# Kernel tuning notes

Measured on AMD Instinct MI355X. Metric: run time of the kernel, lower is better.

The kernel has to match this reference:

```python
import jax, jax.numpy as jnp
import numpy as np

N = 100000
E = 3200000
F_IN, F1, F2, F3, FB, NC = 256, 64, 32, 16, 8, 10


def setup_inputs() -> dict:
    key = jax.random.key(0)
    ks = jax.random.split(key, 12)
    features = jax.random.normal(ks[0], (N, F_IN), dtype=jnp.float32)
    edge_index = jax.random.randint(ks[1], (2, E), 0, N, dtype=jnp.int64)
    def glorot(k, shape):
        lim = np.sqrt(6.0 / (shape[0] + shape[1]))
        return jax.random.uniform(k, shape, jnp.float32, -lim, lim)
    return {
        "features": features,
        "edge_index": edge_index,
        "W1": glorot(ks[2], (F_IN, F1)), "b1": jnp.zeros((F1,), jnp.float32),
        "W2": glorot(ks[3], (F1, F2)),  "b2": jnp.zeros((F2,), jnp.float32),
        "W3": glorot(ks[4], (F2, F3)),  "b3": jnp.zeros((F3,), jnp.float32),
        "Wf": glorot(ks[5], (F3, FB)),  "bf": jnp.zeros((FB,), jnp.float32),
        "Ws": glorot(ks[6], (FB, NC)),  "bs": jnp.zeros((NC,), jnp.float32),
    }


def _gcn_norm(edge_index, n):
    # symmetric normalization with self-loops: deg includes +1 for self-loop
    src, dst = edge_index[0], edge_index[1]
    ones = jnp.ones((edge_index.shape[1],), jnp.float32)
    deg = jax.ops.segment_sum(ones, dst, num_segments=n) + 1.0
    dinv = jax.lax.rsqrt(deg)
    edge_w = dinv[src] * dinv[dst]        # [E]
    self_w = dinv * dinv                   # [N], self-loop weight
    return src, dst, edge_w, self_w


def _gcn_conv(x, W, b, src, dst, edge_w, self_w, n):
    xw = x @ W                                         # [N, Fout]
    msg = xw[src] * edge_w[:, None]                    # gather + scale
    agg = jax.ops.segment_sum(msg, dst, num_segments=n)
    return agg + xw * self_w[:, None] + b


def reference(features, edge_index, W1, b1, W2, b2, W3, b3, Wf, bf, Ws, bs):
    n = features.shape[0]
    src, dst, edge_w, self_w = _gcn_norm(edge_index, n)
    h = jax.nn.relu(_gcn_conv(features, W1, b1, src, dst, edge_w, self_w, n))
    h = jax.nn.relu(_gcn_conv(h, W2, b2, src, dst, edge_w, self_w, n))
    h = jax.nn.relu(_gcn_conv(h, W3, b3, src, dst, edge_w, self_w, n))
    pooled = jnp.mean(h, axis=0, keepdims=True)        # [1, F3]
    hidden = jax.nn.relu(pooled @ Wf + bf)
    scores = hidden @ Ws + bs
    return jax.nn.log_softmax(scores, axis=1)
```

## Files before the change

### kernel.cpp

```cpp
#include <hip/hip_runtime.h>
#include <hip/hip_fp16.h>
#include <math.h>

#define TPB 256
#define BKT_SHIFT 9
#define BKT_N 512
#define NB_MAX 256
#define CHUNK 4096
#define CAP   24576
#define Y_SCALE 16.0f
#define Y_INV_SCALE (1.0f / 16.0f)

typedef short bf16x8 __attribute__((ext_vector_type(8)));
typedef float f32x4  __attribute__((ext_vector_type(4)));

static __device__ inline unsigned short f2bf(float f) {
    union { float f; unsigned u; } v; v.f = f;
    unsigned r = v.u + 0x7FFF + ((v.u >> 16) & 1);
    return (unsigned short)(r >> 16);
}

static __device__ inline unsigned char f2fp8(float x) {
    int p = __builtin_amdgcn_cvt_pk_fp8_f32(x, x, 0, false);
    return (unsigned char)(p & 0xFF);
}

static __device__ inline void acc_word(float* a, unsigned u) {
    a[0] += __builtin_amdgcn_cvt_f32_fp8(u, 0);
    a[1] += __builtin_amdgcn_cvt_f32_fp8(u, 1);
    a[2] += __builtin_amdgcn_cvt_f32_fp8(u, 2);
    a[3] += __builtin_amdgcn_cvt_f32_fp8(u, 3);
}

__global__ __launch_bounds__(256) void setup_kernel(
    const float* __restrict__ W1, unsigned short* __restrict__ Wt1,
    const float* __restrict__ W2, unsigned short* __restrict__ Wt2,
    const float* __restrict__ W3, unsigned short* __restrict__ Wt3,
    int* __restrict__ bcursor, float* __restrict__ pooled, int nbkt)
{
    const int b = blockIdx.x;
    if (b < 16) {
        int base = b * 1024;
        for (int i = base + threadIdx.x; i < base + 1024; i += 256) {
            int k = i / 64, c = i % 64;
            Wt1[c * 256 + k] = f2bf(W1[i]);
        }
    } else if (b < 18) {
        int base = (b - 16) * 1024;
        for (int i = base + threadIdx.x; i < base + 1024; i += 256) {
            int k = i / 32, c = i % 32;
            Wt2[c * 64 + k] = f2bf(W2[i]);
        }
    } else if (b == 18) {
        for (int i = threadIdx.x; i < 512; i += 256) {
            int k = i / 16, c = i % 16;
            Wt3[c * 32 + k] = f2bf(W3[i]);
        }
    } else {
        if (threadIdx.x < nbkt) bcursor[threadIdx.x] = threadIdx.x * CAP;
        if (threadIdx.x < 16) pooled[threadIdx.x] = 0.f;
    }
}

__global__ __launch_bounds__(TPB) void bucket_scatter(
    const int* __restrict__ src, const int* __restrict__ dst,
    int* __restrict__ bcursor, unsigned int* __restrict__ packed, int E, int nbkt)
{
    __shared__ unsigned int  spk[CHUNK];
    __shared__ unsigned char sbk[CHUNK];
    __shared__ int h[NB_MAX];
    __shared__ int base[NB_MAX];
    for (int c0 = blockIdx.x * CHUNK; c0 < E; c0 += gridDim.x * CHUNK) {
        int m = min(CHUNK, E - c0);
        for (int i = threadIdx.x; i < nbkt; i += TPB) h[i] = 0;
        __syncthreads();
        for (int i = threadIdx.x; i < m; i += TPB) {
            int d = dst[c0 + i];
            int s = src[c0 + i];
            int b = d >> BKT_SHIFT;
            spk[i] = ((unsigned)(d & (BKT_N - 1)) << 17) | (unsigned)s;
            sbk[i] = (unsigned char)b;
            atomicAdd(&h[b], 1);
        }
        __syncthreads();
        for (int i = threadIdx.x; i < nbkt; i += TPB) {
            int c = h[i];
            base[i] = c ? atomicAdd(&bcursor[i], c) : 0;
            h[i] = 0;
        }
        __syncthreads();
        for (int i = threadIdx.x; i < m; i += TPB) {
            int b = sbk[i];
            int pos = base[b] + atomicAdd(&h[b], 1);
            packed[pos] = spk[i];
        }
        __syncthreads();
    }
}

__global__ __launch_bounds__(256) void bucket_offsets(
    const int* __restrict__ bcursor, int* __restrict__ boff, int nbkt, int E)
{
    int t = threadIdx.x;
    int v = (t < nbkt) ? (bcursor[t] - t * CAP) : 0;
    __shared__ int tmp[256];
    tmp[t] = v; __syncthreads();
    for (int s = 1; s < 256; s <<= 1) {
        int x = (t >= s) ? tmp[t - s] : 0;
        __syncthreads();
        tmp[t] += x;
        __syncthreads();
    }
    if (t < nbkt) boff[t] = tmp[t] - v;
    if (t == 0) boff[nbkt] = E;
}

__global__ __launch_bounds__(256) void bucket_csr(
    const unsigned int* __restrict__ packed, const int* __restrict__ boff,
    int* __restrict__ off, float* __restrict__ dinv, int* __restrict__ ssrc,
    int n, int nbkt)
{
    const int b   = blockIdx.x;
    const int e0  = boff[b];
    const int cnt = boff[b + 1] - e0;
    const int p0  = b * CAP;
    const int v0  = b << BKT_SHIFT;
    const int nv  = min(BKT_N, n - v0);
    const int t   = threadIdx.x;

    __shared__ int hist[BKT_N];
    __shared__ int cur[BKT_N];
    __shared__ int tmp[256];

    for (int i = t; i < nv; i += 256) hist[i] = 0;
    __syncthreads();
    for (int e = t; e < cnt; e += 256)
        atomicAdd(&hist[packed[p0 + e] >> 17], 1);
    __syncthreads();

    int a = (2 * t     < nv) ? hist[2 * t]     : 0;
    int c = (2 * t + 1 < nv) ? hist[2 * t + 1] : 0;
    int ps = a + c;
    tmp[t] = ps; __syncthreads();
    for (int s = 1; s < 256; s <<= 1) {
        int x = (t >= s) ? tmp[t - s] : 0;
        __syncthreads();
        tmp[t] += x;
        __syncthreads();
    }
    int ex = tmp[t] - ps;
    if (2 * t < nv) {
        cur[2 * t] = ex;
        off[v0 + 2 * t] = e0 + ex;
        dinv[v0 + 2 * t] = rsqrtf((float)a + 1.0f);
    }
    if (2 * t + 1 < nv) {
        cur[2 * t + 1] = ex + a;
        off[v0 + 2 * t + 1] = e0 + ex + a;
        dinv[v0 + 2 * t + 1] = rsqrtf((float)c + 1.0f);
    }
    if (b == nbkt - 1 && t == 0) off[n] = boff[nbkt];
    __syncthreads();

    for (int e = t; e < cnt; e += 256) {
        unsigned p = packed[p0 + e];
        int dl = p >> 17;
        int s  = p & 0x1FFFF;
        int pos = atomicAdd(&cur[dl], 1);
        ssrc[e0 + pos] = s;
    }
}

template<int K, int NCOL, typename AT>
__global__ __launch_bounds__(TPB) void gemm_mfma(
    const AT* __restrict__ A, const unsigned short* __restrict__ Wt,
    const float* __restrict__ dinv, unsigned char* __restrict__ Yq, int n)
{
    constexpr int NT = NCOL / 16;
    constexpr int KS = K / 32;
    const int lane = threadIdx.x & 63;
    const int w    = threadIdx.x >> 6;
    const int rowbase = blockIdx.x * 128 + w * 32;
    const int arow = lane & 15;
    const int kb   = (lane >> 4) * 8;

    f32x4 acc[2][NT];
#pragma unroll
    for (int mt = 0; mt < 2; mt++)
#pragma unroll
        for (int nt = 0; nt < NT; nt++) acc[mt][nt] = (f32x4)(0.f);

#pragma unroll
    for (int ks = 0; ks < KS; ks++) {
        bf16x8 a[2];
#pragma unroll
        for (int mt = 0; mt < 2; mt++) {
            int r = rowbase + mt * 16 + arow;
            if constexpr (sizeof(AT) == 4) {
                if (r < n) {
                    const float4* p = (const float4*)(A + (size_t)r * K + ks * 32 + kb);
                    float4 u = p[0], v = p[1];
                    a[mt][0] = f2bf(u.x); a[mt][1] = f2bf(u.y);
                    a[mt][2] = f2bf(u.z); a[mt][3] = f2bf(u.w);
                    a[mt][4] = f2bf(v.x); a[mt][5] = f2bf(v.y);
                    a[mt][6] = f2bf(v.z); a[mt][7] = f2bf(v.w);
                } else {
#pragma unroll
                    for (int i = 0; i < 8; i++) a[mt][i] = 0;
                }
            } else {
                if (r < n)
                    a[mt] = *(const bf16x8*)(A + (size_t)r * K + ks * 32 + kb);
                else {
#pragma unroll
                    for (int i = 0; i < 8; i++) a[mt][i] = 0;
                }
            }
        }
        bf16x8 b[NT];
#pragma unroll
        for (int nt = 0; nt < NT; nt++)
            b[nt] = *(const bf16x8*)(Wt + (size_t)(nt * 16 + arow) * K + ks * 32 + kb);
#pragma unroll
        for (int mt = 0; mt < 2; mt++)
#pragma unroll
            for (int nt = 0; nt < NT; nt++)
                acc[mt][nt] = __builtin_amdgcn_mfma_f32_16x16x32_bf16(
                    a[mt], b[nt], acc[mt][nt], 0, 0, 0);
    }

#pragma unroll
    for (int mt = 0; mt < 2; mt++) {
        int r0 = rowbase + mt * 16 + (lane >> 4) * 4;
#pragma unroll
        for (int j = 0; j < 4; j++) {
            int r = r0 + j;
            if (r < n) {
                float dv = dinv[r] * Y_SCALE;
#pragma unroll
                for (int nt = 0; nt < NT; nt++)
                    Yq[(size_t)r * NCOL + nt * 16 + arow] = f2fp8(acc[mt][nt][j] * dv);
            }
        }
    }
}

template<int F>
__global__ __launch_bounds__(TPB) void seg_group(
    const int* __restrict__ off, const int* __restrict__ ssrc,
    const unsigned char* __restrict__ Yq, const float* __restrict__ dinv,
    const float* __restrict__ bias, unsigned int* __restrict__ H, int n)
{
    constexpr int G     = F / 16;
    constexpr int LOG2G = (G == 4) ? 2 : 1;
    const int lane  = threadIdx.x & 63;
    const int fl    = lane & (G - 1);
    const int gbase = lane & ~(G - 1);
    const int v     = (blockIdx.x * TPB + threadIdx.x) >> LOG2G;

    if (v >= n) return;

    float acc[16];
#pragma unroll
    for (int i = 0; i < 16; i++) acc[i] = 0.f;

    {
        uint4 q = *(const uint4*)(Yq + (size_t)v * F + fl * 16);
        acc_word(acc + 0, q.x); acc_word(acc + 4, q.y);
        acc_word(acc + 8, q.z); acc_word(acc + 12, q.w);
    }

    const int e0 = off[v], e1 = off[v + 1];
    int e = e0;
    for (; e + G <= e1; e += G) {
        int idx = ssrc[e + fl];
        uint4 q[G];
#pragma unroll
        for (int k = 0; k < G; k++) {
            int sj = __shfl(idx, gbase + k, 64);
            q[k] = *(const uint4*)(Yq + (size_t)sj * F + fl * 16);
        }
#pragma unroll
        for (int k = 0; k < G; k++) {
            acc_word(acc + 0, q[k].x); acc_word(acc + 4, q[k].y);
            acc_word(acc + 8, q[k].z); acc_word(acc + 12, q[k].w);
        }
    }
    int rem = e1 - e;
    if (rem > 0) {
        int idx = (fl < rem) ? ssrc[e + fl] : 0;
        for (int k = 0; k < rem; k++) {
            int sj = __shfl(idx, gbase + k, 64);
            uint4 q = *(const uint4*)(Yq + (size_t)sj * F + fl * 16);
            acc_word(acc + 0, q.x); acc_word(acc + 4, q.y);
            acc_word(acc + 8, q.z); acc_word(acc + 12, q.w);
        }
    }

    float dv = dinv[v] * Y_INV_SCALE;
    unsigned hw[8];
#pragma unroll
    for (int i = 0; i < 16; i += 2) {
        float rx = fmaxf(fmaf(acc[i],     dv, bias[fl * 16 + i]),     0.f);
        float ry = fmaxf(fmaf(acc[i + 1], dv, bias[fl * 16 + i + 1]), 0.f);
        hw[i / 2] = ((unsigned)f2bf(ry) << 16) | (unsigned)f2bf(rx);
    }
    unsigned int* hp = H + (size_t)v * (F / 2) + fl * 8;
    *(uint4*)(hp + 0) = make_uint4(hw[0], hw[1], hw[2], hw[3]);
    *(uint4*)(hp + 4) = make_uint4(hw[4], hw[5], hw[6], hw[7]);
}

__global__ __launch_bounds__(TPB) void seg_pool16(
    const int* __restrict__ off, const int* __restrict__ ssrc,
    const unsigned char* __restrict__ Yq, const float* __restrict__ dinv,
    const float* __restrict__ bias, float* __restrict__ pooled, int n)
{
    constexpr int U = 4;
    const int v = blockIdx.x * TPB + threadIdx.x;

    float r16[16];
#pragma unroll
    for (int i = 0; i < 16; i++) r16[i] = 0.f;

    if (v < n) {
        float acc[16];
#pragma unroll
        for (int i = 0; i < 16; i++) acc[i] = 0.f;

        {
            uint4 q = *(const uint4*)(Yq + (size_t)v * 16);
            acc_word(acc + 0, q.x); acc_word(acc + 4, q.y);
            acc_word(acc + 8, q.z); acc_word(acc + 12, q.w);
        }
        int e0 = off[v], e1 = off[v + 1];
        int e = e0;
        for (; e + U <= e1; e += U) {
            uint4 q[U];
#pragma unroll
            for (int k = 0; k < U; k++)
                q[k] = *(const uint4*)(Yq + (size_t)ssrc[e + k] * 16);
#pragma unroll
            for (int k = 0; k < U; k++) {
                acc_word(acc + 0, q[k].x); acc_word(acc + 4, q[k].y);
                acc_word(acc + 8, q[k].z); acc_word(acc + 12, q[k].w);
            }
        }
        for (; e < e1; e++) {
            uint4 q = *(const uint4*)(Yq + (size_t)ssrc[e] * 16);
            acc_word(acc + 0, q.x); acc_word(acc + 4, q.y);
            acc_word(acc + 8, q.z); acc_word(acc + 12, q.w);
        }

        float dv = dinv[v] * Y_INV_SCALE;
#pragma unroll
        for (int i = 0; i < 16; i++)
            r16[i] = fmaxf(fmaf(acc[i], dv, bias[i]), 0.f);
    }

    __shared__ float red[TPB][17];
#pragma unroll
    for (int i = 0; i < 16; i++) red[threadIdx.x][i] = r16[i];
    __syncthreads();
    for (int st = 128; st >= 1; st >>= 1) {
        if (threadIdx.x < st) {
#pragma unroll
            for (int i = 0; i < 16; i++)
                red[threadIdx.x][i] += red[threadIdx.x + st][i];
        }
        __syncthreads();
    }
    if (threadIdx.x < 16) atomicAdd(&pooled[threadIdx.x], red[0][threadIdx.x]);
}

__global__ void head_kernel(const float* __restrict__ pooled,
                            const float* __restrict__ Wf, const float* __restrict__ bf,
                            const float* __restrict__ Ws, const float* __restrict__ bs,
                            float* __restrict__ out, float invn)
{
    if (threadIdx.x == 0 && blockIdx.x == 0) {
        float p[16], h[8], s[10];
        for (int i = 0; i < 16; i++) p[i] = pooled[i] * invn;
        for (int j = 0; j < 8; j++) {
            float a = bf[j];
            for (int i = 0; i < 16; i++) a = fmaf(p[i], Wf[i * 8 + j], a);
            h[j] = fmaxf(a, 0.f);
        }
        float m = -1e30f;
        for (int c = 0; c < 10; c++) {
            float a = bs[c];
            for (int j = 0; j < 8; j++) a = fmaf(h[j], Ws[j * 10 + c], a);
            s[c] = a;
            m = fmaxf(m, a);
        }
        float lse = 0.f;
        for (int c = 0; c < 10; c++) lse += expf(s[c] - m);
        lse = logf(lse) + m;
        for (int c = 0; c < 10; c++) out[c] = s[c] - lse;
    }
}

static inline size_t align_up(size_t x) { return (x + 255) & ~(size_t)255; }

extern "C" void kernel_launch(void* const* d_in, const int* in_sizes, int n_in,
                              void* d_out, int out_size, void* d_ws, size_t ws_size,
                              hipStream_t stream)
{
    const float* X  = (const float*)d_in[0];
    const int*   ei = (const int*)  d_in[1];
    const float* W1 = (const float*)d_in[2];  const float* b1 = (const float*)d_in[3];
    const float* W2 = (const float*)d_in[4];  const float* b2 = (const float*)d_in[5];
    const float* W3 = (const float*)d_in[6];  const float* b3 = (const float*)d_in[7];
    const float* Wf = (const float*)d_in[8];  const float* bf = (const float*)d_in[9];
    const float* Ws = (const float*)d_in[10]; const float* bs = (const float*)d_in[11];

    const int n = in_sizes[0] / 256;
    const int E = in_sizes[1] / 2;
    const int* src = ei;
    const int* dst = ei + E;
    const int nbkt = (n + BKT_N - 1) / BKT_N;

    char* ws = (char*)d_ws;
    size_t off_b = 0;
    int* bcursor = (int*)(ws + off_b);   off_b += align_up(NB_MAX * 4);
    int* boff    = (int*)(ws + off_b);   off_b += align_up((NB_MAX + 1) * 4);
    float* dinv  = (float*)(ws + off_b); off_b += align_up((size_t)n * 4);
    int* off     = (int*)(ws + off_b);   off_b += align_up((size_t)(n + 1) * 4);
    float* pooled= (float*)(ws + off_b); off_b += align_up(16 * 4);
    unsigned short* Wt1 = (unsigned short*)(ws + off_b); off_b += align_up(64 * 256 * 2);
    unsigned short* Wt2 = (unsigned short*)(ws + off_b); off_b += align_up(32 * 64 * 2);
    unsigned short* Wt3 = (unsigned short*)(ws + off_b); off_b += align_up(16 * 32 * 2);
    unsigned int* packed = (unsigned int*)(ws + off_b); off_b += align_up((size_t)nbkt * CAP * 4);
    int* ssrc    = (int*)(ws + off_b);   off_b += align_up((size_t)E * 4);
    unsigned char* Yq = (unsigned char*)(ws + off_b); off_b += align_up((size_t)n * 64);
    unsigned int* H = (unsigned int*)(ws + off_b); off_b += align_up((size_t)n * 64 * 2);

    setup_kernel<<<20, 256, 0, stream>>>(W1, Wt1, W2, Wt2, W3, Wt3, bcursor, pooled, nbkt);
    int nchunk = (E + CHUNK - 1) / CHUNK;
    bucket_scatter<<<nchunk, TPB, 0, stream>>>(src, dst, bcursor, packed, E, nbkt);
    bucket_offsets<<<1, 256, 0, stream>>>(bcursor, boff, nbkt, E);
    bucket_csr<<<nbkt, 256, 0, stream>>>(packed, boff, off, dinv, ssrc, n, nbkt);

    const int gblk = (n + 127) / 128;
    const int nblk = (n + TPB - 1) / TPB;

    gemm_mfma<256, 64, float><<<gblk, TPB, 0, stream>>>(X, Wt1, dinv, Yq, n);
    seg_group<64><<<(4 * n + TPB - 1) / TPB, TPB, 0, stream>>>(off, ssrc, Yq, dinv, b1, H, n);

    gemm_mfma<64, 32, unsigned short><<<gblk, TPB, 0, stream>>>(
        (const unsigned short*)H, Wt2, dinv, Yq, n);
    seg_group<32><<<(2 * n + TPB - 1) / TPB, TPB, 0, stream>>>(off, ssrc, Yq, dinv, b2, H, n);

    gemm_mfma<32, 16, unsigned short><<<gblk, TPB, 0, stream>>>(
        (const unsigned short*)H, Wt3, dinv, Yq, n);
    seg_pool16<<<nblk, TPB, 0, stream>>>(off, ssrc, Yq, dinv, b3, pooled, n);

    head_kernel<<<1, 64, 0, stream>>>(pooled, Wf, bf, Ws, bs, (float*)d_out, 1.0f / (float)n);
}
```

Baseline: 256.3 us.

## Fold bucket offset scan into bucket_csr and deepen gather unrolling

Removes the single-block bucket_offsets kernel: each bucket_csr block now recomputes the prefix scan over bucket counts itself and derives its edge range and the final off[n]. This saves a kernel launch and a dependency step at the cost of a redundant 256-wide scan per block. Separately, seg_group gains a 2G-wide main loop that issues twice as many outstanding gathers before accumulating, and seg_pool16's unroll factor goes from 4 to 8. Both raise memory-level parallelism on the edge gathers but may increase register pressure.

```diff
diff --git a/kernel.cpp b/kernel.cpp
--- a/kernel.cpp
+++ b/kernel.cpp
@@ -98,35 +98,30 @@
     }
 }
 
-__global__ __launch_bounds__(256) void bucket_offsets(
-    const int* __restrict__ bcursor, int* __restrict__ boff, int nbkt, int E)
-{
-    int t = threadIdx.x;
-    int v = (t < nbkt) ? (bcursor[t] - t * CAP) : 0;
-    __shared__ int tmp[256];
-    tmp[t] = v; __syncthreads();
-    for (int s = 1; s < 256; s <<= 1) {
-        int x = (t >= s) ? tmp[t - s] : 0;
-        __syncthreads();
-        tmp[t] += x;
-        __syncthreads();
-    }
-    if (t < nbkt) boff[t] = tmp[t] - v;
-    if (t == 0) boff[nbkt] = E;
-}
-
 __global__ __launch_bounds__(256) void bucket_csr(
-    const unsigned int* __restrict__ packed, const int* __restrict__ boff,
+    const unsigned int* __restrict__ packed, const int* __restrict__ bcursor,
     int* __restrict__ off, float* __restrict__ dinv, int* __restrict__ ssrc,
     int n, int nbkt)
 {
-    const int b   = blockIdx.x;
-    const int e0  = boff[b];
-    const int cnt = boff[b + 1] - e0;
-    const int p0  = b * CAP;
-    const int v0  = b << BKT_SHIFT;
-    const int nv  = min(BKT_N, n - v0);
-    const int t   = threadIdx.x;
+    const int b  = blockIdx.x;
+    const int t  = threadIdx.x;
+    const int p0 = b * CAP;
+    const int v0 = b << BKT_SHIFT;
+    const int nv = min(BKT_N, n - v0);
+
+    __shared__ int stmp[256];
+    int cval = (t < nbkt) ? (bcursor[t] - t * CAP) : 0;
+    stmp[t] = cval; __syncthreads();
+    for (int s = 1; s < 256; s <<= 1) {
+        int x = (t >= s) ? stmp[t - s] : 0;
+        __syncthreads();
+        stmp[t] += x;
+        __syncthreads();
+    }
+    const int e0  = (b == 0) ? 0 : stmp[b - 1];
+    const int cnt = stmp[b] - e0;
+    if (b == nbkt - 1 && t == 0) off[n] = stmp[nbkt - 1];
+    __syncthreads();
 
     __shared__ int hist[BKT_N];
     __shared__ int cur[BKT_N];
@@ -159,7 +154,6 @@
         off[v0 + 2 * t + 1] = e0 + ex + a;
         dinv[v0 + 2 * t + 1] = rsqrtf((float)c + 1.0f);
     }
-    if (b == nbkt - 1 && t == 0) off[n] = boff[nbkt];
     __syncthreads();
 
     for (int e = t; e < cnt; e += 256) {
@@ -272,6 +266,26 @@
 
     const int e0 = off[v], e1 = off[v + 1];
     int e = e0;
+    for (; e + 2 * G <= e1; e += 2 * G) {
+        int idx0 = ssrc[e + fl];
+        int idx1 = ssrc[e + G + fl];
+        uint4 q[2 * G];
+#pragma unroll
+        for (int k = 0; k < G; k++) {
+            int sj = __shfl(idx0, gbase + k, 64);
+            q[k] = *(const uint4*)(Yq + (size_t)sj * F + fl * 16);
+        }
+#pragma unroll
+        for (int k = 0; k < G; k++) {
+            int sj = __shfl(idx1, gbase + k, 64);
+            q[G + k] = *(const uint4*)(Yq + (size_t)sj * F + fl * 16);
+        }
+#pragma unroll
+        for (int k = 0; k < 2 * G; k++) {
+            acc_word(acc + 0, q[k].x); acc_word(acc + 4, q[k].y);
+            acc_word(acc + 8, q[k].z); acc_word(acc + 12, q[k].w);
+        }
+    }
     for (; e + G <= e1; e += G) {
         int idx = ssrc[e + fl];
         uint4 q[G];
@@ -315,7 +329,7 @@
     const unsigned char* __restrict__ Yq, const float* __restrict__ dinv,
     const float* __restrict__ bias, float* __restrict__ pooled, int n)
 {
-    constexpr int U = 4;
+    constexpr int U = 8;
     const int v = blockIdx.x * TPB + threadIdx.x;
 
     float r16[16];
@@ -422,7 +436,6 @@
     char* ws = (char*)d_ws;
     size_t off_b = 0;
     int* bcursor = (int*)(ws + off_b);   off_b += align_up(NB_MAX * 4);
-    int* boff    = (int*)(ws + off_b);   off_b += align_up((NB_MAX + 1) * 4);
     float* dinv  = (float*)(ws + off_b); off_b += align_up((size_t)n * 4);
     int* off     = (int*)(ws + off_b);   off_b += align_up((size_t)(n + 1) * 4);
     float* pooled= (float*)(ws + off_b); off_b += align_up(16 * 4);
@@ -437,8 +450,7 @@
     setup_kernel<<<20, 256, 0, stream>>>(W1, Wt1, W2, Wt2, W3, Wt3, bcursor, pooled, nbkt);
     int nchunk = (E + CHUNK - 1) / CHUNK;
     bucket_scatter<<<nchunk, TPB, 0, stream>>>(src, dst, bcursor, packed, E, nbkt);
-    bucket_offsets<<<1, 256, 0, stream>>>(bcursor, boff, nbkt, E);
-    bucket_csr<<<nbkt, 256, 0, stream>>>(packed, boff, off, dinv, ssrc, n, nbkt);
+    bucket_csr<<<nbkt, 256, 0, stream>>>(packed, bcursor, off, dinv, ssrc, n, nbkt);
 
     const int gblk = (n + 127) / 128;
     const int nblk = (n + TPB - 1) / TPB;
```

Result: faster. 245.4 us, median of 2 (-4.2%).
